# Kernel optimization log

Measured on AMD Instinct MI355X. Metric: run time of the kernel, lower is better.

## Reference

```python
import jax, jax.numpy as jnp
import numpy as np

B, C, L = 8, 256, 2048      # batch, res_channels, seq_len
E = 2 * C                    # attention / S4 width = 512
CH = 4                       # S4 channels
SQRT_HALF = 0.7071067811865476


def setup_inputs() -> dict:
    key = jax.random.key(0)
    ks = jax.random.split(key, 12)
    def n(k, s, sc):
        return jax.random.normal(k, s, dtype=jnp.float32) * sc
    return dict(
        x=jax.random.normal(ks[0], (B, C, L), dtype=jnp.float32),
        original=jax.random.normal(ks[1], (B, C, L), dtype=jnp.float32),
        sn_scale=jnp.ones((1, C, 1), jnp.float32),
        conv_w=n(ks[2], (E, C, 3), 0.05), conv_b=jnp.zeros((E,), jnp.float32),
        s4_ln_g=jnp.ones((E,), jnp.float32), s4_ln_b=jnp.zeros((E,), jnp.float32),
        s4_kernel=n(ks[3], (CH, E, L), 0.01),           # long-conv kernel per channel
        s4_D=n(ks[4], (CH, E), 1.0),                     # skip connection D
        s4_out_w=n(ks[5], (E, CH * E), 0.02), s4_out_b=jnp.zeros((E,), jnp.float32),
        attn_v_w=n(ks[6], (E, E), 0.02), attn_v_b=jnp.zeros((E,), jnp.float32),
        attn_o_w=n(ks[7], (E, E), 0.02), attn_o_b=jnp.zeros((E,), jnp.float32),
        res_w=n(ks[8], (C, C, 1), 0.05), res_b=jnp.zeros((C,), jnp.float32),
        skip_w=n(ks[9], (C, C, 1), 0.05), skip_b=jnp.zeros((C,), jnp.float32),
    )


def reference(x, original, sn_scale, conv_w, conv_b, s4_ln_g, s4_ln_b,
              s4_kernel, s4_D, s4_out_w, s4_out_b,
              attn_v_w, attn_v_b, attn_o_w, attn_o_b,
              res_w, res_b, skip_w, skip_b):
    eps = 1e-8
    # RMSNorm over channel dim (dim=1)
    rms = jnp.sqrt(jnp.sum(x * x, axis=1, keepdims=True)) / np.sqrt(x.shape[1]).astype(np.float32)
    x_n = sn_scale * x / (rms + eps)
    # h = x + original (pre-norm x), conv k=3 pad=1, GELU
    h = x + original
    h = jax.lax.conv_general_dilated(h, conv_w, (1,), [(1, 1)],
                                     dimension_numbers=('NCH', 'OIH', 'NCH'))
    h = jax.nn.gelu(h + conv_b[None, :, None], approximate=False)
    # --- S4 / GConv: LN over channels, FFT causal long conv, D-skip, GELU, out linear ---
    mu = h.mean(axis=1, keepdims=True)
    var = h.var(axis=1, keepdims=True)
    u = (h - mu) / jnp.sqrt(var + 1e-5) * s4_ln_g[None, :, None] + s4_ln_b[None, :, None]
    n2 = 2 * u.shape[-1]
    uf = jnp.fft.rfft(u, n=n2)                      # (B, E, F)
    kf = jnp.fft.rfft(s4_kernel, n=n2)              # (CH, E, F)
    y = jnp.fft.irfft(jnp.einsum('bhf,chf->bchf', uf, kf), n=n2)[..., :u.shape[-1]]
    y = y + s4_D[None, :, :, None] * u[:, None]     # (B, CH, E, L)
    y = jax.nn.gelu(y.reshape(y.shape[0], CH * E, y.shape[-1]), approximate=False)
    h_t = jnp.einsum('oc,bcl->bol', s4_out_w, y) + s4_out_b[None, :, None]  # (B, E, L)
    # --- local-window MHA with window_size=1: each position attends only to itself,
    # softmax over a single unmasked score == 1, so out = Wo @ (Wv @ x + bv) + bo exactly ---
    v = jnp.einsum('oe,bel->bol', attn_v_w, h_t) + attn_v_b[None, :, None]
    h_s = jnp.einsum('oe,bel->bol', attn_o_w, v) + attn_o_b[None, :, None]
    h2 = h_t + h_s
    out = jnp.tanh(h2[:, :C]) * jax.nn.sigmoid(h2[:, C:])
    res = jnp.einsum('oc,bcl->bol', res_w[:, :, 0], out) + res_b[None, :, None]
    skip = jnp.einsum('oc,bcl->bol', skip_w[:, :, 0], out) + skip_b[None, :, None]
    return ((x_n + res) * SQRT_HALF, skip)
```

## Files before the change

### kernel.cpp

```cpp
#include <hip/hip_runtime.h>
#include <hip/hip_bf16.h>
#include <math.h>

typedef __attribute__((ext_vector_type(8))) short short8;
typedef __attribute__((ext_vector_type(4))) float float4_t;
typedef __attribute__((ext_vector_type(2))) float cf2;
typedef unsigned short ushort_t;

#define NBL 16384

#define WS_CONVA   ((size_t)0)
#define WS_WV      ((size_t)786432)
#define WS_WO      ((size_t)1310720)
#define WS_W1      ((size_t)1835008)
#define WS_WCAT    ((size_t)3932160)
#define WS_A2      ((size_t)4194304)
#define WS_ACOMB   ((size_t)4718592)
#define WS_BCOMB   ((size_t)6815744)
#define WS_XN      ((size_t)6819840)
#define WS_H0PT    ((size_t)23597056)
#define WS_U       ((size_t)31993856)
#define WS_UF      ((size_t)65548288)
#define WS_KF      ((size_t)99102720)
#define WS_G       ((size_t)132657152)
#define WS_UB      ((size_t)208162816)
#define WS_GT      WS_UF
#define WS_H2      WS_G
#define WS_GATET   (WS_G + 25165824)

__device__ __forceinline__ float gelu_f(float x) {
    float t = x * x;
    float a2 = x * fmaf(0.07135481627f, t, 1.59576912161f);
    return x / (1.f + __expf(-a2));
}
__device__ __forceinline__ float tanh_f(float a) {
    return 1.f - 2.f / (1.f + __expf(2.f * a));
}
__device__ __forceinline__ float sigmoid_f(float b) {
    return 1.f / (1.f + __expf(-b));
}

__device__ __forceinline__ unsigned int pack_bf2(float a, float b) {
    __hip_bfloat16 ha = __float2bfloat16(a), hb = __float2bfloat16(b);
    unsigned short ua = *(unsigned short*)&ha, ub = *(unsigned short*)&hb;
    return (unsigned int)ua | ((unsigned int)ub << 16);
}
__device__ __forceinline__ cf2 unpack_c(unsigned int v) {
    cf2 r;
    r.x = __uint_as_float(v << 16);
    r.y = __uint_as_float(v & 0xffff0000u);
    return r;
}
__device__ __forceinline__ float bf2f(ushort_t u) {
    return __uint_as_float(((unsigned int)u) << 16);
}

__device__ __forceinline__ cf2 cswap(cf2 a) { return __builtin_shufflevector(a, a, 1, 0); }
template<int SGN>
__device__ __forceinline__ cf2 cmuli(cf2 a) {
    cf2 s = cswap(a);
    return s * cf2{(float)(-SGN), (float)SGN};
}
__device__ __forceinline__ cf2 cmul(cf2 a, cf2 b) {
    cf2 t = cswap(a) * cf2{-b.y, b.y};
    return a * cf2{b.x, b.x} + t;
}
__device__ __forceinline__ cf2 cmulc(cf2 a, float wr, float wi) {
    cf2 t = cswap(a) * cf2{-wi, wi};
    return a * cf2{wr, wr} + t;
}

__global__ __launch_bounds__(256) void wprep_kernel(
    const float* __restrict__ conv_w, const float* __restrict__ attn_v_w,
    const float* __restrict__ attn_o_w, const float* __restrict__ s4_out_w,
    const float* __restrict__ res_w, const float* __restrict__ skip_w,
    __hip_bfloat16* __restrict__ convA, __hip_bfloat16* __restrict__ WvT,
    __hip_bfloat16* __restrict__ WoBf, __hip_bfloat16* __restrict__ W1T,
    __hip_bfloat16* __restrict__ Wcat)
{
    const int N0 = 393216, N1 = 655360, N2c = 917504, N3 = 1966080, N4 = 2097152;
    for (int i = blockIdx.x * 256 + threadIdx.x; i < N4; i += gridDim.x * 256) {
        if (i < N0) {
            int m = i / 768, r = i - m * 768, dk = r >> 8, c = r & 255;
            convA[i] = __float2bfloat16(conv_w[m * 768 + c * 3 + dk]);
        } else if (i < N1) {
            int j = i - N0; int row = j >> 9, e = j & 511;
            WvT[j] = __float2bfloat16(attn_v_w[e * 512 + row]);
        } else if (i < N2c) {
            WoBf[i - N1] = __float2bfloat16(attn_o_w[i - N1]);
        } else if (i < N3) {
            int j = i - N2c; int ck = j >> 9, e = j & 511;
            W1T[j] = __float2bfloat16(s4_out_w[e * 2048 + ck]);
        } else {
            int j = i - N3; int m = j >> 8, c = j & 255;
            float v = (m < 256) ? res_w[m * 256 + c] : skip_w[(m - 256) * 256 + c];
            Wcat[j] = __float2bfloat16(v);
        }
    }
}

__global__ __launch_bounds__(256) void bias2_kernel(
    const __hip_bfloat16* __restrict__ A2, const float* __restrict__ s4_out_b,
    const float* __restrict__ attn_o_w, const float* __restrict__ attn_v_b,
    const float* __restrict__ attn_o_b, float* __restrict__ bcomb)
{
    __shared__ float red[256];
    int o = blockIdx.x, t = threadIdx.x;
    float s = 0.f;
    for (int e = t; e < 512; e += 256)
        s += __bfloat162float(A2[o * 512 + e]) * s4_out_b[e] + attn_o_w[o * 512 + e] * attn_v_b[e];
    red[t] = s; __syncthreads();
    for (int k = 128; k > 0; k >>= 1) { if (t < k) red[t] += red[t + k]; __syncthreads(); }
    if (t == 0) bcomb[o] = red[0] + attn_o_b[o];
}

__global__ __launch_bounds__(512) void prep_kernel(
    const float* __restrict__ x, const float* __restrict__ orig,
    const float* __restrict__ sn, ushort_t* __restrict__ xnb, ushort_t* __restrict__ h0pT)
{
    __shared__ float red[8][64];
    __shared__ ushort_t T[256 * 66];
    int blk = blockIdx.x, t = threadIdx.x;
    int lane = t & 63, cg = t >> 6;
    int b = blk >> 5, l0 = (blk & 31) << 6;
    size_t basein = (size_t)b * 524288 + l0 + lane;
    float ss = 0.f;
    for (int c = cg; c < 256; c += 8) {
        size_t idx = basein + (size_t)c * 2048;
        float xv = x[idx], ov = orig[idx];
        ss += xv * xv;
        __hip_bfloat16 hv = __float2bfloat16(xv + ov);
        T[c * 66 + lane] = *(ushort_t*)&hv;
    }
    red[cg][lane] = ss;
    __syncthreads();
    float tot = 0.f;
    #pragma unroll
    for (int k = 0; k < 8; ++k) tot += red[k][lane];
    float inv = 1.0f / (sqrtf(tot) * 0.0625f + 1e-8f);
    __hip_bfloat16* xo = (__hip_bfloat16*)xnb;
    for (int c = cg; c < 256; c += 8) {
        size_t idx = basein + (size_t)c * 2048;
        xo[idx] = __float2bfloat16(sn[c] * x[idx] * inv);
    }
    int c2 = t & 255, half = t >> 8;
    size_t rowbase = (size_t)(b * 2050 + 1 + l0);
    for (int r = half; r < 64; r += 2)
        h0pT[(rowbase + r) * 256 + c2] = T[c2 * 66 + r];
    if ((blk & 31) == 0) {
        if (t < 256) h0pT[(size_t)(b * 2050) * 256 + t] = 0;
        else         h0pT[(size_t)(b * 2050 + 2049) * 256 + (t - 256)] = 0;
    }
}

__global__ __launch_bounds__(256) void transpose_kernel(
    const ushort_t* __restrict__ in, ushort_t* __restrict__ out, int R, int C)
{
    __shared__ ushort_t S[64 * 65];
    int c0 = blockIdx.x * 64, r0 = blockIdx.y * 64;
    int t = threadIdx.x, lx = t & 63, ly0 = t >> 6;
    #pragma unroll
    for (int ly = ly0; ly < 64; ly += 4) {
        int r = r0 + ly, c = c0 + lx;
        S[ly * 65 + lx] = (r < R && c < C) ? in[(size_t)r * C + c] : (ushort_t)0;
    }
    __syncthreads();
    #pragma unroll
    for (int ly = ly0; ly < 64; ly += 4) {
        int oc = c0 + ly, orr = r0 + lx;
        if (oc < C && orr < R) out[(size_t)oc * R + orr] = S[lx * 65 + ly];
    }
}

__global__ __launch_bounds__(512) void ln_kernel(
    const ushort_t* __restrict__ h, ushort_t* __restrict__ ub,
    const float* __restrict__ gam, const float* __restrict__ bet)
{
    __shared__ float r1[8][64], r2[8][64];
    int blk = blockIdx.x, t = threadIdx.x;
    int lane = t & 63, og = t >> 6;
    int n = (blk << 6) + lane;
    float s1 = 0.f, s2 = 0.f;
    for (int o = og; o < 512; o += 8) { float v = bf2f(h[(size_t)o * NBL + n]); s1 += v; s2 += v * v; }
    r1[og][lane] = s1; r2[og][lane] = s2;
    __syncthreads();
    float mu = 0.f, m2 = 0.f;
    #pragma unroll
    for (int k = 0; k < 8; ++k) { mu += r1[k][lane]; m2 += r2[k][lane]; }
    mu *= (1.f / 512.f); m2 *= (1.f / 512.f);
    float rstd = rsqrtf(m2 - mu * mu + 1e-5f);
    __hip_bfloat16* ubb = (__hip_bfloat16*)ub;
    for (int o = og; o < 512; o += 8) {
        size_t idx = (size_t)o * NBL + n;
        ubb[idx] = __float2bfloat16((bf2f(h[idx]) - mu) * rstd * gam[o] + bet[o]);
    }
}

#define PERM(m) ((((m) & 3) << 2) | ((m) >> 2))

template<int SGN>
__device__ __forceinline__ void dft4p(cf2& a0, cf2& a1, cf2& a2, cf2& a3) {
    cf2 t0 = a0 + a2, t1 = a0 - a2, t2 = a1 + a3, t3 = a1 - a3;
    cf2 j3 = cmuli<SGN>(t3);
    a0 = t0 + t2; a2 = t0 - t2;
    a1 = t1 + j3; a3 = t1 - j3;
}
template<int SGN>
__device__ __forceinline__ void dft4p_half(cf2& a0, cf2& a1, cf2& a2, cf2& a3) {
    cf2 u0 = a0, u1 = a1;
    cf2 j1 = cmuli<SGN>(u1);
    a0 = u0 + u1; a2 = u0 - u1;
    a1 = u0 + j1; a3 = u0 - j1;
}
template<int SGN>
__device__ __forceinline__ void dft4p_out01(cf2 a0, cf2 a1, cf2 a2, cf2 a3, cf2& o0, cf2& o1) {
    cf2 t0 = a0 + a2, t1 = a0 - a2, t2 = a1 + a3, t3 = a1 - a3;
    o0 = t0 + t2;
    o1 = t1 + cmuli<SGN>(t3);
}

template<int SGN>
__device__ __forceinline__ void dft16_stepB(cf2* x) {
    const float sg = (float)SGN;
    const float C16[10] = {1.f, 0.92387953f, 0.70710678f, 0.38268343f, 0.f,
                           -0.38268343f, -0.70710678f, -0.92387953f, -1.f, -0.92387953f};
    const float S16[10] = {0.f, 0.38268343f, 0.70710678f, 0.92387953f, 1.f,
                           0.92387953f, 0.70710678f, 0.38268343f, 0.f, -0.38268343f};
    #pragma unroll
    for (int s = 1; s < 4; ++s)
        #pragma unroll
        for (int r = 1; r < 4; ++r) {
            int e = s * r;
            x[4 * s + r] = cmulc(x[4 * s + r], C16[e], sg * S16[e]);
        }
}
template<int SGN>
__device__ __forceinline__ void dft16p(cf2* x) {
    #pragma unroll
    for (int r = 0; r < 4; ++r) dft4p<SGN>(x[r], x[4 + r], x[8 + r], x[12 + r]);
    dft16_stepB<SGN>(x);
    #pragma unroll
    for (int s = 0; s < 4; ++s) dft4p<SGN>(x[4 * s], x[4 * s + 1], x[4 * s + 2], x[4 * s + 3]);
}
template<int SGN>
__device__ __forceinline__ void dft16_halfin(cf2* x) {
    #pragma unroll
    for (int r = 0; r < 4; ++r) dft4p_half<SGN>(x[r], x[4 + r], x[8 + r], x[12 + r]);
    dft16_stepB<SGN>(x);
    #pragma unroll
    for (int s = 0; s < 4; ++s) dft4p<SGN>(x[4 * s], x[4 * s + 1], x[4 * s + 2], x[4 * s + 3]);
}
template<int SGN>
__device__ __forceinline__ void dft16_halfout(cf2* x, cf2* y) {
    #pragma unroll
    for (int r = 0; r < 4; ++r) dft4p<SGN>(x[r], x[4 + r], x[8 + r], x[12 + r]);
    dft16_stepB<SGN>(x);
    #pragma unroll
    for (int s = 0; s < 4; ++s)
        dft4p_out01<SGN>(x[4 * s], x[4 * s + 1], x[4 * s + 2], x[4 * s + 3], y[s], y[4 + s]);
}

template<int SGN>
__device__ __forceinline__ void tw_after(cf2* x, float p, float invQ) {
    float s1, c1; __sincosf((float)SGN * 6.283185307179586f * p * invQ, &s1, &c1);
    cf2 w1 = {c1, s1}, w = w1;
    #pragma unroll
    for (int m = 1; m < 16; ++m) { x[PERM(m)] = cmul(x[PERM(m)], w); w = cmul(w, w1); }
}
template<int SGN>
__device__ __forceinline__ void tw_before(cf2* x, float p, float invQ) {
    float s1, c1; __sincosf((float)SGN * 6.283185307179586f * p * invQ, &s1, &c1);
    cf2 w1 = {c1, s1}, w = w1;
    #pragma unroll
    for (int j = 1; j < 16; ++j) { x[j] = cmul(x[j], w); w = cmul(w, w1); }
}

__global__ __launch_bounds__(256) void fft_fwd_kernel(
    const ushort_t* __restrict__ ubf, const float* __restrict__ s4k,
    uint4* __restrict__ uf, uint4* __restrict__ kf)
{
    __shared__ cf2 S[4368];
    int wg = blockIdx.x, t = threadIdx.x;
    cf2 x[16];
    if (wg < 2048) {
        int bp = wg >> 9, e = wg & 511;
        const ushort_t* p0 = ubf + (size_t)e * NBL + (size_t)bp * 4096;
        #pragma unroll
        for (int j = 0; j < 8; ++j) {
            int i = j * 256 + t;
            x[j] = cf2{bf2f(p0[i]), bf2f(p0[i + 2048])};
        }
    } else {
        const float* p0 = s4k + (size_t)(wg - 2048) * 2048;
        #pragma unroll
        for (int j = 0; j < 8; ++j) x[j] = cf2{p0[j * 256 + t], 0.f};
    }
    dft16_halfin<-1>(x);
    tw_after<-1>(x, (float)t, 1.f / 4096.f);
    int tb = 17 * (t >> 4) + (t & 15);
    #pragma unroll
    for (int m = 0; m < 16; ++m) S[tb + 273 * m] = x[PERM(m)];
    __syncthreads();
    int b2 = 273 * (t >> 4) + (t & 15);
    #pragma unroll
    for (int j = 0; j < 16; ++j) x[j] = S[b2 + 17 * j];
    dft16p<-1>(x);
    tw_after<-1>(x, (float)(t & 15), 1.f / 256.f);
    #pragma unroll
    for (int m = 0; m < 16; ++m) S[b2 + 17 * m] = x[PERM(m)];
    __syncthreads();
    int b3 = 273 * (t >> 4) + 17 * (t & 15);
    #pragma unroll
    for (int j = 0; j < 16; ++j) x[j] = S[b3 + j];
    dft16p<-1>(x);
    const float sc = (wg < 2048) ? 1.f : (1.f / 4096.f);
    uint4* dst = ((wg < 2048) ? (uf + (size_t)wg * 1024) : (kf + (size_t)(wg - 2048) * 1024)) + 4 * t;
    #pragma unroll
    for (int q = 0; q < 4; ++q) {
        uint4 o;
        cf2 v0 = x[PERM(4 * q)] * sc, v1 = x[PERM(4 * q + 1)] * sc;
        cf2 v2 = x[PERM(4 * q + 2)] * sc, v3 = x[PERM(4 * q + 3)] * sc;
        o.x = pack_bf2(v0.x, v0.y);
        o.y = pack_bf2(v1.x, v1.y);
        o.z = pack_bf2(v2.x, v2.y);
        o.w = pack_bf2(v3.x, v3.y);
        dst[q] = o;
    }
}

__global__ __launch_bounds__(256) void fft_inv_kernel(
    const uint4* __restrict__ uf, const uint4* __restrict__ kf,
    const ushort_t* __restrict__ ubf, const float* __restrict__ s4D,
    ushort_t* __restrict__ g)
{
    __shared__ cf2 S[4368];
    int wg = blockIdx.x, t = threadIdx.x;
    int bp = wg >> 11, ch = (wg >> 9) & 3, e = wg & 511;
    const uint4* zr = uf + (size_t)(bp * 512 + e) * 1024 + 4 * t;
    const uint4* kr = kf + (size_t)(ch * 512 + e) * 1024 + 4 * t;
    cf2 x[16];
    #pragma unroll
    for (int q = 0; q < 4; ++q) {
        uint4 a4 = zr[q], b4 = kr[q];
        x[4 * q + 0] = cmul(unpack_c(a4.x), unpack_c(b4.x));
        x[4 * q + 1] = cmul(unpack_c(a4.y), unpack_c(b4.y));
        x[4 * q + 2] = cmul(unpack_c(a4.z), unpack_c(b4.z));
        x[4 * q + 3] = cmul(unpack_c(a4.w), unpack_c(b4.w));
    }
    dft16p<1>(x);
    int b1 = 273 * (t >> 4) + 17 * (t & 15);
    #pragma unroll
    for (int m = 0; m < 16; ++m) S[b1 + m] = x[PERM(m)];
    __syncthreads();
    int b2 = 273 * (t >> 4) + (t & 15);
    #pragma unroll
    for (int j = 0; j < 16; ++j) x[j] = S[b2 + 17 * j];
    tw_before<1>(x, (float)(t & 15), 1.f / 256.f);
    dft16p<1>(x);
    #pragma unroll
    for (int m = 0; m < 16; ++m) S[b2 + 17 * m] = x[PERM(m)];
    __syncthreads();
    int b3 = 17 * (t >> 4) + (t & 15);
    #pragma unroll
    for (int j = 0; j < 16; ++j) x[j] = S[b3 + 273 * j];
    tw_before<1>(x, (float)t, 1.f / 4096.f);
    cf2 y[8];
    dft16_halfout<1>(x, y);
    float dD = s4D[ch * 512 + e];
    const ushort_t* ub = ubf + (size_t)e * NBL + (size_t)bp * 4096;
    __hip_bfloat16* go = (__hip_bfloat16*)g + ((size_t)(ch * 512 + e) * NBL + (size_t)bp * 4096);
    #pragma unroll
    for (int m = 0; m < 8; ++m) {
        int l = m * 256 + t;
        go[l]        = __float2bfloat16(gelu_f(fmaf(dD, bf2f(ub[l]), y[m].x)));
        go[l + 2048] = __float2bfloat16(gelu_f(fmaf(dD, bf2f(ub[l + 2048]), y[m].y)));
    }
}

template<int BSRC, int EPI>
__global__ __launch_bounds__(256) void gemm_kernel(
    const ushort_t* __restrict__ A, const ushort_t* __restrict__ Bm,
    ushort_t* __restrict__ Cb, float* __restrict__ Cf,
    int M, int N, int K,
    const float* __restrict__ bias, const float* __restrict__ bias2,
    const ushort_t* __restrict__ xnb, float* __restrict__ dout)
{
    __shared__ ushort_t Alds[128 * 40];
    __shared__ ushort_t Blds[128 * 40];
    const int t = threadIdx.x;
    const int n0 = blockIdx.x * 128, m0 = blockIdx.y * 128;
    const int w = t >> 6, lane = t & 63, quad = lane >> 4, lr = lane & 15;
    const int wm = (w >> 1) * 64, wn = (w & 1) * 64;

    const int i_s = t >> 1, j0 = (t & 1) * 16;
    int bI = 0, lI = 0;
    if (BSRC == 1) { int n = n0 + i_s; bI = n >> 11; lI = n & 2047; }

    float4_t acc[4][4];
    #pragma unroll
    for (int i = 0; i < 4; ++i)
        #pragma unroll
        for (int j = 0; j < 4; ++j) { float4_t z = {0.f, 0.f, 0.f, 0.f}; acc[i][j] = z; }

    short8 pa0, pa1, pb0, pb1;
    {
        const short8* sa = (const short8*)(A + (size_t)(m0 + i_s) * K + j0);
        pa0 = sa[0]; pa1 = sa[1];
        const ushort_t* sp;
        if (BSRC == 0) sp = Bm + (size_t)(n0 + i_s) * K + j0;
        else           sp = Bm + (size_t)(bI * 2050 + lI) * 256 + j0;
        const short8* sb = (const short8*)sp;
        pb0 = sb[0]; pb1 = sb[1];
    }

    for (int kt = 0; kt < K; kt += 32) {
        if (kt) __syncthreads();
        *(short8*)&Alds[i_s * 40 + j0]     = pa0;
        *(short8*)&Alds[i_s * 40 + j0 + 8] = pa1;
        *(short8*)&Blds[i_s * 40 + j0]     = pb0;
        *(short8*)&Blds[i_s * 40 + j0 + 8] = pb1;
        __syncthreads();
        int kn = kt + 32;
        if (kn < K) {
            const short8* sa = (const short8*)(A + (size_t)(m0 + i_s) * K + kn + j0);
            pa0 = sa[0]; pa1 = sa[1];
            const ushort_t* sp;
            if (BSRC == 0) sp = Bm + (size_t)(n0 + i_s) * K + kn + j0;
            else { int dk = kn >> 8, cb = kn & 255; sp = Bm + (size_t)(bI * 2050 + lI + dk) * 256 + cb + j0; }
            const short8* sb = (const short8*)sp;
            pb0 = sb[0]; pb1 = sb[1];
        }
        short8 af[4], bfr[4];
        #pragma unroll
        for (int im = 0; im < 4; ++im)
            af[im] = *(const short8*)&Alds[(wm + im * 16 + lr) * 40 + quad * 8];
        #pragma unroll
        for (int in_ = 0; in_ < 4; ++in_)
            bfr[in_] = *(const short8*)&Blds[(wn + in_ * 16 + lr) * 40 + quad * 8];
        #pragma unroll
        for (int im = 0; im < 4; ++im)
            #pragma unroll
            for (int in_ = 0; in_ < 4; ++in_)
                acc[im][in_] = __builtin_amdgcn_mfma_f32_16x16x32_bf16(af[im], bfr[in_], acc[im][in_], 0, 0, 0);
    }

    #pragma unroll
    for (int im = 0; im < 4; ++im) {
        #pragma unroll
        for (int in_ = 0; in_ < 4; ++in_) {
            int n = n0 + wn + in_ * 16 + lr;
            int mb = m0 + wm + im * 16 + quad * 4;
            #pragma unroll
            for (int r = 0; r < 4; ++r) {
                int m = mb + r;
                float v = acc[im][in_][r];
                if (EPI == 0) {
                    v += bias[m];
                    ((__hip_bfloat16*)Cb)[(size_t)m * N + n] = __float2bfloat16(gelu_f(v));
                } else if (EPI == 1) {
                    v += (m == n) ? 1.0f : 0.0f;
                    ((__hip_bfloat16*)Cb)[(size_t)m * N + n] = __float2bfloat16(v);
                } else if (EPI == 2) {
                    ((__hip_bfloat16*)Cb)[(size_t)m * N + n] = __float2bfloat16(v);
                } else if (EPI == 3) {
                    v += bias[m];
                    ((__hip_bfloat16*)Cb)[(size_t)m * N + n] = __float2bfloat16(v);
                } else {
                    int bb = n >> 11, ll = n & 2047;
                    if (m < 256) {
                        v += bias[m];
                        int idx = (bb << 19) + (m << 11) + ll;
                        dout[idx] = (bf2f(xnb[idx]) + v) * 0.70710678118654752f;
                    } else {
                        v += bias2[m - 256];
                        dout[4194304 + (bb << 19) + ((m - 256) << 11) + ll] = v;
                    }
                }
            }
        }
    }
}

__global__ __launch_bounds__(256) void gate_t_kernel(
    const ushort_t* __restrict__ h2, ushort_t* __restrict__ gateT)
{
    __shared__ ushort_t S[64 * 65];
    int n0 = blockIdx.x * 64, m0 = blockIdx.y * 64;
    int t = threadIdx.x, lx = t & 63, ly0 = t >> 6;
    const __hip_bfloat16* h2b = (const __hip_bfloat16*)h2;
    #pragma unroll
    for (int ly = ly0; ly < 64; ly += 4) {
        float a = __bfloat162float(h2b[(size_t)(m0 + ly) * NBL + n0 + lx]);
        float b = __bfloat162float(h2b[(size_t)(m0 + 256 + ly) * NBL + n0 + lx]);
        __hip_bfloat16 v = __float2bfloat16(tanh_f(a) * sigmoid_f(b));
        S[ly * 65 + lx] = *(ushort_t*)&v;
    }
    __syncthreads();
    #pragma unroll
    for (int ly = ly0; ly < 64; ly += 4)
        gateT[(size_t)(n0 + ly) * 256 + m0 + lx] = S[lx * 65 + ly];
}

extern "C" void kernel_launch(void* const* d_in, const int* in_sizes, int n_in,
                              void* d_out, int out_size, void* d_ws, size_t ws_size,
                              hipStream_t stream)
{
    const float* x         = (const float*)d_in[0];
    const float* original  = (const float*)d_in[1];
    const float* sn_scale  = (const float*)d_in[2];
    const float* conv_w    = (const float*)d_in[3];
    const float* conv_b    = (const float*)d_in[4];
    const float* s4_ln_g   = (const float*)d_in[5];
    const float* s4_ln_b   = (const float*)d_in[6];
    const float* s4_kernel = (const float*)d_in[7];
    const float* s4_D      = (const float*)d_in[8];
    const float* s4_out_w  = (const float*)d_in[9];
    const float* s4_out_b  = (const float*)d_in[10];
    const float* attn_v_w  = (const float*)d_in[11];
    const float* attn_v_b  = (const float*)d_in[12];
    const float* attn_o_w  = (const float*)d_in[13];
    const float* attn_o_b  = (const float*)d_in[14];
    const float* res_w     = (const float*)d_in[15];
    const float* res_b     = (const float*)d_in[16];
    const float* skip_w    = (const float*)d_in[17];
    const float* skip_b    = (const float*)d_in[18];

    char* ws = (char*)d_ws;
    __hip_bfloat16* convA = (__hip_bfloat16*)(ws + WS_CONVA);
    __hip_bfloat16* WvT   = (__hip_bfloat16*)(ws + WS_WV);
    __hip_bfloat16* WoBf  = (__hip_bfloat16*)(ws + WS_WO);
    __hip_bfloat16* W1T   = (__hip_bfloat16*)(ws + WS_W1);
    __hip_bfloat16* Wcat  = (__hip_bfloat16*)(ws + WS_WCAT);
    ushort_t* A2    = (ushort_t*)(ws + WS_A2);
    ushort_t* Acomb = (ushort_t*)(ws + WS_ACOMB);
    float* bcombp  = (float*)(ws + WS_BCOMB);
    ushort_t* xnb  = (ushort_t*)(ws + WS_XN);
    ushort_t* h0pT = (ushort_t*)(ws + WS_H0PT);
    ushort_t* hP   = (ushort_t*)(ws + WS_U);
    ushort_t* ubP  = (ushort_t*)(ws + WS_UB);
    uint4* ufP = (uint4*)(ws + WS_UF);
    uint4* kfP = (uint4*)(ws + WS_KF);
    ushort_t* gP    = (ushort_t*)(ws + WS_G);
    ushort_t* gT    = (ushort_t*)(ws + WS_GT);
    ushort_t* h2P   = (ushort_t*)(ws + WS_H2);
    ushort_t* gateT = (ushort_t*)(ws + WS_GATET);

    wprep_kernel<<<dim3(4096), dim3(256), 0, stream>>>(conv_w, attn_v_w, attn_o_w, s4_out_w,
        res_w, skip_w, convA, WvT, WoBf, W1T, Wcat);
    gemm_kernel<0, 1><<<dim3(4, 4), dim3(256), 0, stream>>>(
        (const ushort_t*)WoBf, (const ushort_t*)WvT, A2, nullptr, 512, 512, 512,
        nullptr, nullptr, nullptr, nullptr);
    bias2_kernel<<<dim3(512), dim3(256), 0, stream>>>(
        (const __hip_bfloat16*)A2, s4_out_b, attn_o_w, attn_v_b, attn_o_b, bcombp);
    gemm_kernel<0, 2><<<dim3(16, 4), dim3(256), 0, stream>>>(
        A2, (const ushort_t*)W1T, Acomb, nullptr, 512, 2048, 512,
        nullptr, nullptr, nullptr, nullptr);

    prep_kernel<<<dim3(256), dim3(512), 0, stream>>>(x, original, sn_scale, xnb, h0pT);
    gemm_kernel<1, 0><<<dim3(128, 4), dim3(256), 0, stream>>>(
        (const ushort_t*)convA, h0pT, hP, nullptr, 512, NBL, 768,
        conv_b, nullptr, nullptr, nullptr);
    ln_kernel<<<dim3(256), dim3(512), 0, stream>>>(hP, ubP, s4_ln_g, s4_ln_b);
    fft_fwd_kernel<<<dim3(4096), dim3(256), 0, stream>>>(ubP, s4_kernel, ufP, kfP);
    fft_inv_kernel<<<dim3(8192), dim3(256), 0, stream>>>(ufP, kfP, ubP, s4_D, gP);
    transpose_kernel<<<dim3(256, 32), dim3(256), 0, stream>>>(gP, gT, 2048, 16384);
    gemm_kernel<0, 3><<<dim3(128, 4), dim3(256), 0, stream>>>(
        (const ushort_t*)Acomb, gT, h2P, nullptr, 512, NBL, 2048,
        bcombp, nullptr, nullptr, nullptr);
    gate_t_kernel<<<dim3(256, 4), dim3(256), 0, stream>>>(h2P, gateT);
    gemm_kernel<0, 4><<<dim3(128, 4), dim3(256), 0, stream>>>(
        (const ushort_t*)Wcat, gateT, nullptr, nullptr, 512, NBL, 256,
        res_b, skip_b, xnb, (float*)d_out);
}
```

Baseline: 440.8 us.

## Fuse D-skip/GELU into transpose and tanh-sigmoid gate into GEMM epilogue

The LN output is stored with batch pairs interleaved, so the forward FFT loads packed 32-bit pairs and the inverse FFT writes raw packed bf16 outputs with no D-skip or GELU. A new gdt kernel applies the D-skip and GELU while transposing into the GEMM B layout, replacing the separate transpose. The gate GEMM now permutes A rows so each block holds matching tanh and sigmoid channel halves and applies the gate in an LDS epilogue, which removes the h2 round trip and the gate_t kernel. Packed bf16 conversion via a builtin is used where available. The cost is more complex indexing and an extra LDS staging pass in the GEMM epilogue.

```diff
diff --git a/kernel.cpp b/kernel.cpp
--- a/kernel.cpp
+++ b/kernel.cpp
@@ -6,6 +6,7 @@
 typedef __attribute__((ext_vector_type(4))) float float4_t;
 typedef __attribute__((ext_vector_type(2))) float cf2;
 typedef unsigned short ushort_t;
+typedef unsigned int uint_t;
 
 #define NBL 16384
 
@@ -20,13 +21,12 @@
 #define WS_XN      ((size_t)6819840)
 #define WS_H0PT    ((size_t)23597056)
 #define WS_U       ((size_t)31993856)
-#define WS_UF      ((size_t)65548288)
+#define WS_GT      ((size_t)65548288)
+#define WS_UF      WS_GT
 #define WS_KF      ((size_t)99102720)
 #define WS_G       ((size_t)132657152)
+#define WS_GATET   (WS_G + 25165824)
 #define WS_UB      ((size_t)208162816)
-#define WS_GT      WS_UF
-#define WS_H2      WS_G
-#define WS_GATET   (WS_G + 25165824)
 
 __device__ __forceinline__ float gelu_f(float x) {
     float t = x * x;
@@ -41,9 +41,18 @@
 }
 
 __device__ __forceinline__ unsigned int pack_bf2(float a, float b) {
+#if __has_builtin(__builtin_amdgcn_cvt_pk_bf16_f32)
+    auto v = __builtin_amdgcn_cvt_pk_bf16_f32(a, b);
+    unsigned int r; __builtin_memcpy(&r, &v, 4); return r;
+#else
     __hip_bfloat16 ha = __float2bfloat16(a), hb = __float2bfloat16(b);
     unsigned short ua = *(unsigned short*)&ha, ub = *(unsigned short*)&hb;
     return (unsigned int)ua | ((unsigned int)ub << 16);
+#endif
+}
+__device__ __forceinline__ ushort_t f2bfu(float a) {
+    __hip_bfloat16 h = __float2bfloat16(a);
+    return *(ushort_t*)&h;
 }
 __device__ __forceinline__ cf2 unpack_c(unsigned int v) {
     cf2 r;
@@ -129,8 +138,7 @@
         size_t idx = basein + (size_t)c * 2048;
         float xv = x[idx], ov = orig[idx];
         ss += xv * xv;
-        __hip_bfloat16 hv = __float2bfloat16(xv + ov);
-        T[c * 66 + lane] = *(ushort_t*)&hv;
+        T[c * 66 + lane] = f2bfu(xv + ov);
     }
     red[cg][lane] = ss;
     __syncthreads();
@@ -150,25 +158,6 @@
     if ((blk & 31) == 0) {
         if (t < 256) h0pT[(size_t)(b * 2050) * 256 + t] = 0;
         else         h0pT[(size_t)(b * 2050 + 2049) * 256 + (t - 256)] = 0;
-    }
-}
-
-__global__ __launch_bounds__(256) void transpose_kernel(
-    const ushort_t* __restrict__ in, ushort_t* __restrict__ out, int R, int C)
-{
-    __shared__ ushort_t S[64 * 65];
-    int c0 = blockIdx.x * 64, r0 = blockIdx.y * 64;
-    int t = threadIdx.x, lx = t & 63, ly0 = t >> 6;
-    #pragma unroll
-    for (int ly = ly0; ly < 64; ly += 4) {
-        int r = r0 + ly, c = c0 + lx;
-        S[ly * 65 + lx] = (r < R && c < C) ? in[(size_t)r * C + c] : (ushort_t)0;
-    }
-    __syncthreads();
-    #pragma unroll
-    for (int ly = ly0; ly < 64; ly += 4) {
-        int oc = c0 + ly, orr = r0 + lx;
-        if (oc < C && orr < R) out[(size_t)oc * R + orr] = S[lx * 65 + ly];
     }
 }
 
@@ -189,10 +178,11 @@
     for (int k = 0; k < 8; ++k) { mu += r1[k][lane]; m2 += r2[k][lane]; }
     mu *= (1.f / 512.f); m2 *= (1.f / 512.f);
     float rstd = rsqrtf(m2 - mu * mu + 1e-5f);
-    __hip_bfloat16* ubb = (__hip_bfloat16*)ub;
+    int b = n >> 11, l = n & 2047;
+    size_t sbase = (size_t)(b >> 1) * 4096 + 2 * l + (b & 1);
     for (int o = og; o < 512; o += 8) {
         size_t idx = (size_t)o * NBL + n;
-        ubb[idx] = __float2bfloat16((bf2f(h[idx]) - mu) * rstd * gam[o] + bet[o]);
+        ub[(size_t)o * 16384 + sbase] = f2bfu((bf2f(h[idx]) - mu) * rstd * gam[o] + bet[o]);
     }
 }
 
@@ -284,12 +274,9 @@
     cf2 x[16];
     if (wg < 2048) {
         int bp = wg >> 9, e = wg & 511;
-        const ushort_t* p0 = ubf + (size_t)e * NBL + (size_t)bp * 4096;
-        #pragma unroll
-        for (int j = 0; j < 8; ++j) {
-            int i = j * 256 + t;
-            x[j] = cf2{bf2f(p0[i]), bf2f(p0[i + 2048])};
-        }
+        const unsigned int* p0 = (const unsigned int*)ubf + (size_t)e * 8192 + (size_t)bp * 2048;
+        #pragma unroll
+        for (int j = 0; j < 8; ++j) x[j] = unpack_c(p0[j * 256 + t]);
     } else {
         const float* p0 = s4k + (size_t)(wg - 2048) * 2048;
         #pragma unroll
@@ -330,8 +317,7 @@
 
 __global__ __launch_bounds__(256) void fft_inv_kernel(
     const uint4* __restrict__ uf, const uint4* __restrict__ kf,
-    const ushort_t* __restrict__ ubf, const float* __restrict__ s4D,
-    ushort_t* __restrict__ g)
+    unsigned int* __restrict__ g2)
 {
     __shared__ cf2 S[4368];
     int wg = blockIdx.x, t = threadIdx.x;
@@ -366,14 +352,38 @@
     tw_before<1>(x, (float)t, 1.f / 4096.f);
     cf2 y[8];
     dft16_halfout<1>(x, y);
-    float dD = s4D[ch * 512 + e];
-    const ushort_t* ub = ubf + (size_t)e * NBL + (size_t)bp * 4096;
-    __hip_bfloat16* go = (__hip_bfloat16*)g + ((size_t)(ch * 512 + e) * NBL + (size_t)bp * 4096);
-    #pragma unroll
-    for (int m = 0; m < 8; ++m) {
-        int l = m * 256 + t;
-        go[l]        = __float2bfloat16(gelu_f(fmaf(dD, bf2f(ub[l]), y[m].x)));
-        go[l + 2048] = __float2bfloat16(gelu_f(fmaf(dD, bf2f(ub[l + 2048]), y[m].y)));
+    unsigned int* go = g2 + (size_t)(ch * 512 + e) * 8192 + (size_t)bp * 2048;
+    #pragma unroll
+    for (int m = 0; m < 8; ++m)
+        go[m * 256 + t] = pack_bf2(y[m].x, y[m].y);
+}
+
+__global__ __launch_bounds__(256) void gdt_kernel(
+    const unsigned int* __restrict__ g2, const unsigned int* __restrict__ ub2,
+    const float* __restrict__ s4D, ushort_t* __restrict__ gT)
+{
+    __shared__ unsigned int S2[64 * 65];
+    int c0 = blockIdx.x * 64, r0 = blockIdx.y * 64;
+    int t = threadIdx.x, lx = t & 63, ly0 = t >> 6;
+    #pragma unroll
+    for (int ly = ly0; ly < 64; ly += 4) {
+        int r = r0 + ly, cp = c0 + lx;
+        cf2 y2 = unpack_c(g2[(size_t)r * 8192 + cp]);
+        cf2 u2 = unpack_c(ub2[(size_t)(r & 511) * 8192 + cp]);
+        float d = s4D[r];
+        float v0 = gelu_f(fmaf(d, u2.x, y2.x));
+        float v1 = gelu_f(fmaf(d, u2.y, y2.y));
+        S2[ly * 65 + lx] = pack_bf2(v0, v1);
+    }
+    __syncthreads();
+    #pragma unroll
+    for (int ly = ly0; ly < 64; ly += 4) {
+        int oc = c0 + ly;
+        unsigned int v = S2[lx * 65 + ly];
+        int bp = oc >> 11, l = oc & 2047;
+        size_t na = (size_t)(bp * 4096 + l) * 2048 + r0 + lx;
+        gT[na] = (ushort_t)(v & 0xffff);
+        gT[na + 4194304] = (ushort_t)(v >> 16);
     }
 }
 
@@ -385,14 +395,17 @@
     const float* __restrict__ bias, const float* __restrict__ bias2,
     const ushort_t* __restrict__ xnb, float* __restrict__ dout)
 {
-    __shared__ ushort_t Alds[128 * 40];
-    __shared__ ushort_t Blds[128 * 40];
+    __shared__ ushort_t SM[10240];
+    ushort_t* Alds = SM;
+    ushort_t* Blds = SM + 5120;
     const int t = threadIdx.x;
     const int n0 = blockIdx.x * 128, m0 = blockIdx.y * 128;
     const int w = t >> 6, lane = t & 63, quad = lane >> 4, lr = lane & 15;
     const int wm = (w >> 1) * 64, wn = (w & 1) * 64;
 
     const int i_s = t >> 1, j0 = (t & 1) * 16;
+    int a_row = m0 + i_s;
+    if (EPI == 5) a_row = (i_s < 64) ? (64 * blockIdx.y + i_s) : (192 + 64 * blockIdx.y + i_s);
     int bI = 0, lI = 0;
     if (BSRC == 1) { int n = n0 + i_s; bI = n >> 11; lI = n & 2047; }
 
@@ -404,7 +417,7 @@
 
     short8 pa0, pa1, pb0, pb1;
     {
-        const short8* sa = (const short8*)(A + (size_t)(m0 + i_s) * K + j0);
+        const short8* sa = (const short8*)(A + (size_t)a_row * K + j0);
         pa0 = sa[0]; pa1 = sa[1];
         const ushort_t* sp;
         if (BSRC == 0) sp = Bm + (size_t)(n0 + i_s) * K + j0;
@@ -422,7 +435,7 @@
         __syncthreads();
         int kn = kt + 32;
         if (kn < K) {
-            const short8* sa = (const short8*)(A + (size_t)(m0 + i_s) * K + kn + j0);
+            const short8* sa = (const short8*)(A + (size_t)a_row * K + kn + j0);
             pa0 = sa[0]; pa1 = sa[1];
             const ushort_t* sp;
             if (BSRC == 0) sp = Bm + (size_t)(n0 + i_s) * K + kn + j0;
@@ -442,6 +455,44 @@
             #pragma unroll
             for (int in_ = 0; in_ < 4; ++in_)
                 acc[im][in_] = __builtin_amdgcn_mfma_f32_16x16x32_bf16(af[im], bfr[in_], acc[im][in_], 0, 0, 0);
+    }
+
+    if (EPI == 5) {
+        const int by = blockIdx.y;
+        __syncthreads();
+        #pragma unroll
+        for (int p = 0; p < 2; ++p) {
+            if (p) __syncthreads();
+            if ((w & 1) == p) {
+                #pragma unroll
+                for (int im = 0; im < 4; ++im)
+                    #pragma unroll
+                    for (int in_ = 0; in_ < 4; ++in_) {
+                        int nl = in_ * 16 + lr;
+                        #pragma unroll
+                        for (int r = 0; r < 4; ++r) {
+                            int i = wm + im * 16 + quad * 4 + r;
+                            int me = (i < 64) ? (64 * by + i) : (192 + 64 * by + i);
+                            SM[i * 68 + nl] = f2bfu(acc[im][in_][r] + bias[me]);
+                        }
+                    }
+            }
+            __syncthreads();
+            int nl = t >> 2, gcb = (t & 3) * 16;
+            size_t obase = (size_t)(n0 + 64 * p + nl) * 256 + 64 * by + gcb;
+            short8 o0, o1;
+            #pragma unroll
+            for (int j = 0; j < 16; ++j) {
+                int gc = gcb + j;
+                float a = bf2f(SM[gc * 68 + nl]);
+                float bb = bf2f(SM[(gc + 64) * 68 + nl]);
+                ushort_t gv = f2bfu(tanh_f(a) * sigmoid_f(bb));
+                if (j < 8) o0[j] = (short)gv; else o1[j - 8] = (short)gv;
+            }
+            *(short8*)(Cb + obase) = o0;
+            *(short8*)(Cb + obase + 8) = o1;
+        }
+        return;
     }
 
     #pragma unroll
@@ -462,9 +513,6 @@
                     ((__hip_bfloat16*)Cb)[(size_t)m * N + n] = __float2bfloat16(v);
                 } else if (EPI == 2) {
                     ((__hip_bfloat16*)Cb)[(size_t)m * N + n] = __float2bfloat16(v);
-                } else if (EPI == 3) {
-                    v += bias[m];
-                    ((__hip_bfloat16*)Cb)[(size_t)m * N + n] = __float2bfloat16(v);
                 } else {
                     int bb = n >> 11, ll = n & 2047;
                     if (m < 256) {
@@ -479,26 +527,6 @@
             }
         }
     }
-}
-
-__global__ __launch_bounds__(256) void gate_t_kernel(
-    const ushort_t* __restrict__ h2, ushort_t* __restrict__ gateT)
-{
-    __shared__ ushort_t S[64 * 65];
-    int n0 = blockIdx.x * 64, m0 = blockIdx.y * 64;
-    int t = threadIdx.x, lx = t & 63, ly0 = t >> 6;
-    const __hip_bfloat16* h2b = (const __hip_bfloat16*)h2;
-    #pragma unroll
-    for (int ly = ly0; ly < 64; ly += 4) {
-        float a = __bfloat162float(h2b[(size_t)(m0 + ly) * NBL + n0 + lx]);
-        float b = __bfloat162float(h2b[(size_t)(m0 + 256 + ly) * NBL + n0 + lx]);
-        __hip_bfloat16 v = __float2bfloat16(tanh_f(a) * sigmoid_f(b));
-        S[ly * 65 + lx] = *(ushort_t*)&v;
-    }
-    __syncthreads();
-    #pragma unroll
-    for (int ly = ly0; ly < 64; ly += 4)
-        gateT[(size_t)(n0 + ly) * 256 + m0 + lx] = S[lx * 65 + ly];
 }
 
 extern "C" void kernel_launch(void* const* d_in, const int* in_sizes, int n_in,
@@ -540,9 +568,8 @@
     ushort_t* ubP  = (ushort_t*)(ws + WS_UB);
     uint4* ufP = (uint4*)(ws + WS_UF);
     uint4* kfP = (uint4*)(ws + WS_KF);
-    ushort_t* gP    = (ushort_t*)(ws + WS_G);
+    unsigned int* g2P = (unsigned int*)(ws + WS_G);
     ushort_t* gT    = (ushort_t*)(ws + WS_GT);
-    ushort_t* h2P   = (ushort_t*)(ws + WS_H2);
     ushort_t* gateT = (ushort_t*)(ws + WS_GATET);
 
     wprep_kernel<<<dim3(4096), dim3(256), 0, stream>>>(conv_w, attn_v_w, attn_o_w, s4_out_w,
@@ -562,12 +589,12 @@
         conv_b, nullptr, nullptr, nullptr);
     ln_kernel<<<dim3(256), dim3(512), 0, stream>>>(hP, ubP, s4_ln_g, s4_ln_b);
     fft_fwd_kernel<<<dim3(4096), dim3(256), 0, stream>>>(ubP, s4_kernel, ufP, kfP);
-    fft_inv_kernel<<<dim3(8192), dim3(256), 0, stream>>>(ufP, kfP, ubP, s4_D, gP);
-    transpose_kernel<<<dim3(256, 32), dim3(256), 0, stream>>>(gP, gT, 2048, 16384);
-    gemm_kernel<0, 3><<<dim3(128, 4), dim3(256), 0, stream>>>(
-        (const ushort_t*)Acomb, gT, h2P, nullptr, 512, NBL, 2048,
+    fft_inv_kernel<<<dim3(8192), dim3(256), 0, stream>>>(ufP, kfP, g2P);
+    gdt_kernel<<<dim3(128, 32), dim3(256), 0, stream>>>(
+        g2P, (const unsigned int*)ubP, s4_D, gT);
+    gemm_kernel<0, 5><<<dim3(128, 4), dim3(256), 0, stream>>>(
+        (const ushort_t*)Acomb, gT, gateT, nullptr, 512, NBL, 2048,
         bcombp, nullptr, nullptr, nullptr);
-    gate_t_kernel<<<dim3(256, 4), dim3(256), 0, stream>>>(h2P, gateT);
     gemm_kernel<0, 4><<<dim3(128, 4), dim3(256), 0, stream>>>(
         (const ushort_t*)Wcat, gateT, nullptr, nullptr, 512, NBL, 256,
         res_b, skip_b, xnb, (float*)d_out);
```

Result: faster. 421.8 us (-4.3%).
